# Performance work log

Measured on AMD Instinct MI355X. Metric: run time of the kernel, lower is better.

Reference implementation:

```python
import jax, jax.numpy as jnp
import numpy as np
from jax import lax

B, S, H, V, J, K = 8, 512, 768, 35004, 30, 9
PAD = 0

def setup_inputs() -> dict:
    key = jax.random.key(0)
    ks = jax.random.split(key, 12)
    std = 0.02
    return {
        'x': jax.random.randint(ks[0], (B, S), 0, V),
        'decoder_input': jax.random.normal(ks[1], (B, J, H), jnp.float32),
        'encoder_output': jax.random.normal(ks[2], (B, S, H), jnp.float32),
        'hidden': jax.random.normal(ks[3], (1, B, H), jnp.float32),
        'teacher': jax.random.randint(ks[4], (B, J, K), 0, V),
        'max_len': K,
        'embed': jax.random.normal(ks[5], (V, H), jnp.float32) * std,
        'w_ih': jax.random.normal(ks[6], (3 * H, H), jnp.float32) * std,
        'w_hh': jax.random.normal(ks[7], (3 * H, H), jnp.float32) * std,
        'b_ih': jnp.zeros((3 * H,), jnp.float32),
        'b_hh': jnp.zeros((3 * H,), jnp.float32),
        'wg_w': jax.random.normal(ks[8], (1, 3 * H), jnp.float32) * std,
        'wg_b': jnp.zeros((1,), jnp.float32),
    }

def gru_cell(w, h, w_ih, w_hh, b_ih, b_hh):
    # PyTorch GRU gate order: reset, update, new
    gi = w @ w_ih.T + b_ih          # [B,3H]
    gh = h @ w_hh.T + b_hh          # [B,3H]
    ir, iz, inn = jnp.split(gi, 3, axis=-1)
    hr, hz, hn = jnp.split(gh, 3, axis=-1)
    r = jax.nn.sigmoid(ir + hr)
    z = jax.nn.sigmoid(iz + hz)
    n = jnp.tanh(inn + r * hn)
    return (1.0 - z) * n + z * h

def reference(x, decoder_input, encoder_output, hidden, teacher, max_len,
              embed, w_ih, w_hh, b_ih, b_hh, wg_w, wg_b):
    mask = (x == PAD)                      # [B,S]
    batch_ix = jnp.arange(x.shape[0])[:, None]

    def tok_step(carry, teach_t):
        w, h = carry                       # w,h: [B,H]; teach_t: [B]
        h = gru_cell(w, h, w_ih, w_hh, b_ih, b_hh)
        logits_hist = jnp.einsum('bsh,bh->bs', encoder_output, h)
        logits_hist = jnp.where(mask, -1e9, logits_hist)
        a_hist = jax.nn.softmax(logits_hist, axis=-1)          # [B,S]
        a_vocab = jax.nn.softmax(h @ embed.T, axis=-1)         # [B,V]
        context = jnp.einsum('bs,bsh->bh', a_hist, encoder_output)
        p_gen = jax.nn.sigmoid(
            jnp.concatenate([w, h, context], axis=-1) @ wg_w.T + wg_b)  # [B,1]
        p_ctx = jnp.zeros_like(a_vocab).at[batch_ix, x].add(a_hist)     # scatter_add pointer copy
        p_final = p_gen * a_vocab + (1.0 - p_gen) * p_ctx
        w_next = embed[teach_t]            # teacher forcing (dropout omitted: eval mode)
        return (w_next, h), p_final

    def slot_step(h, slot_in):
        w0, teach_j = slot_in              # w0: [B,H]; teach_j: [K,B]
        (_, h), p = lax.scan(tok_step, (w0, h), teach_j)
        return h, p                        # p: [K,B,V]

    h0 = hidden[0]                                      # [B,H]
    slots = jnp.swapaxes(decoder_input, 0, 1)           # [J,B,H]
    teach = jnp.transpose(teacher, (1, 2, 0))           # [J,K,B]
    _, outs = lax.scan(slot_step, h0, (slots, teach))   # [J,K,B,V]
    return jnp.transpose(outs, (2, 0, 1, 3))            # [B,J,K,V]
```

## Files before the change

### kernel.cpp

```cpp
#include <hip/hip_runtime.h>
#include <hip/hip_bf16.h>

typedef _Float16 f16;
typedef _Float16 f16x8 __attribute__((ext_vector_type(8)));
typedef _Float16 h2 __attribute__((ext_vector_type(2)));
typedef float f32x4 __attribute__((ext_vector_type(4)));
typedef unsigned ui4v __attribute__((ext_vector_type(4)));
typedef unsigned long long ull;

#define B_ 8
#define S_ 512
#define H_ 768
#define V_ 35004
#define J_ 30
#define K_ 9
#define R_ 2160
#define H3 2304
#define CBLK 24
#define CUPB 32


__global__ void k_zero(int* p, int n) {
    int i = blockIdx.x * 256 + threadIdx.x;
    if (i < n) p[i] = 0;
}

__global__ void k_cast(const float* __restrict__ s, f16* __restrict__ d, long n) {
    for (long i = (long)blockIdx.x * 256 + threadIdx.x; i < n; i += (long)gridDim.x * 256)
        d[i] = (f16)s[i];
}

__global__ void k_build_wall(const float* __restrict__ emb, const float* __restrict__ dec,
                             const int* __restrict__ teacher, f16* __restrict__ Wall) {
    int r = blockIdx.x;
    int b = r / 270, s = r % 270, j = s / 9, t = s % 9;
    const float* src = (t == 0) ? dec + ((long)b * J_ + j) * H_
                                : emb + (long)teacher[((long)b * J_ + j) * K_ + (t - 1)] * H_;
    f16* dst = Wall + (long)r * H_;
    for (int c = threadIdx.x; c < H_; c += 256) dst[c] = (f16)src[c];
}

__global__ void k_build_enc(const float* __restrict__ enc, f16* __restrict__ ehi,
                            f16* __restrict__ elo, f16* __restrict__ encT) {
    long n = (long)B_ * S_ * H_;
    for (long i = (long)blockIdx.x * 256 + threadIdx.x; i < n; i += (long)gridDim.x * 256) {
        float v = enc[i];
        f16 hi = (f16)v;
        ehi[i] = hi;
        elo[i] = (f16)(v - (float)hi);
        int h = (int)(i % H_);
        long bs = i / H_;
        int s = (int)(bs % S_), b = (int)(bs / S_);
        encT[((long)b * H_ + h) * S_ + s] = hi;
    }
}

__global__ void k_init_h(const float* __restrict__ hidden, ull* __restrict__ hbuf) {
    int i = blockIdx.x * 256 + threadIdx.x;
    if (i < B_ * H_) {
        int b = i / H_, u = i % H_;
        hbuf[(long)b * 1536 + u] = (ull)__float_as_uint(hidden[i]);
    }
}

typedef const __attribute__((address_space(1))) unsigned GASU;
typedef __attribute__((address_space(3))) unsigned LASU;
__device__ __forceinline__ void gld16(const f16* g, f16* l) {
    __builtin_amdgcn_global_load_lds((GASU*)g, (LASU*)l, 16, 0, 0);
}

template <int MODE>
__global__ __launch_bounds__(256) void k_gemm(const f16* __restrict__ A, const f16* __restrict__ Bm,
                                              float* __restrict__ C, const float* __restrict__ bias,
                                              int M, int N, int K, long sA, long sB, long sC,
                                              float* __restrict__ psum) {
    A += (long)blockIdx.z * sA;
    Bm += (long)blockIdx.z * sB;
    C += (long)blockIdx.z * sC;
    const int m0 = blockIdx.y * 128, n0 = blockIdx.x * 128;
    __shared__ f16 As[128 * 32];
    __shared__ f16 Bs[128 * 32];
    __shared__ float rpart[2][128];
    const int tid = threadIdx.x, lane = tid & 63, wave = tid >> 6;
    const int wm = wave >> 1, wn = wave & 1;
    const int fr = lane & 15, kg = lane >> 4;
    f32x4 acc[4][4] = {};
    const int idxu = wave * 128;
    const int i0 = idxu + lane, i1 = idxu + 64 + lane;
    const int r0 = i0 >> 2, k80 = i0 & 3;
    const int r1 = i1 >> 2, k81 = i1 & 3;
    int ga0 = m0 + r0; if (ga0 >= M) ga0 = M - 1;
    int ga1 = m0 + r1; if (ga1 >= M) ga1 = M - 1;
    int gb0 = n0 + r0; if (gb0 >= N) gb0 = N - 1;
    int gb1 = n0 + r1; if (gb1 >= N) gb1 = N - 1;
    const f16* pa0 = A + (long)ga0 * K + k80 * 8;
    const f16* pa1 = A + (long)ga1 * K + k81 * 8;
    const f16* pb0 = Bm + (long)gb0 * K + k80 * 8;
    const f16* pb1 = Bm + (long)gb1 * K + k81 * 8;
    for (int kt = 0; kt < K; kt += 32) {
        gld16(pa0 + kt, As + idxu * 8);
        gld16(pa1 + kt, As + idxu * 8 + 512);
        gld16(pb0 + kt, Bs + idxu * 8);
        gld16(pb1 + kt, Bs + idxu * 8 + 512);
        __syncthreads();
        f16x8 af[4], bf[4];
#pragma unroll
        for (int m = 0; m < 4; ++m) af[m] = *(const f16x8*)(As + (wm * 64 + m * 16 + fr) * 32 + kg * 8);
#pragma unroll
        for (int n = 0; n < 4; ++n) bf[n] = *(const f16x8*)(Bs + (wn * 64 + n * 16 + fr) * 32 + kg * 8);
#pragma unroll
        for (int m = 0; m < 4; ++m)
#pragma unroll
            for (int n = 0; n < 4; ++n)
                acc[m][n] = __builtin_amdgcn_mfma_f32_16x16x32_f16(af[m], bf[n], acc[m][n], 0, 0, 0);
        __syncthreads();
    }
    const int crow = m0 + wm * 64 + (lane >> 4) * 4;
    const int ccol = n0 + wn * 64 + fr;
    if (MODE == 3) {
        float rs[4][4];
#pragma unroll
        for (int m = 0; m < 4; ++m)
#pragma unroll
            for (int q = 0; q < 4; ++q) rs[m][q] = 0.f;
#pragma unroll
        for (int n = 0; n < 4; ++n) {
            int col = ccol + n * 16;
            if (col >= N) continue;
#pragma unroll
            for (int m = 0; m < 4; ++m) {
#pragma unroll
                for (int q = 0; q < 4; ++q) {
                    int row = crow + m * 16 + q;
                    if (row < M) {
                        float e = __expf(acc[m][n][q]);
                        C[(long)row * N + col] = e;
                        rs[m][q] += e;
                    }
                }
            }
        }
#pragma unroll
        for (int m = 0; m < 4; ++m)
#pragma unroll
            for (int q = 0; q < 4; ++q) {
                float v = rs[m][q];
                v += __shfl_xor(v, 1);
                v += __shfl_xor(v, 2);
                v += __shfl_xor(v, 4);
                v += __shfl_xor(v, 8);
                rs[m][q] = v;
            }
        if ((lane & 15) == 0) {
#pragma unroll
            for (int m = 0; m < 4; ++m)
#pragma unroll
                for (int q = 0; q < 4; ++q)
                    rpart[wn][wm * 64 + (lane >> 4) * 4 + m * 16 + q] = rs[m][q];
        }
        __syncthreads();
        if (tid < 128) {
            int row = m0 + tid;
            if (row < M) psum[(long)blockIdx.x * M + row] = rpart[0][tid] + rpart[1][tid];
        }
    } else {
#pragma unroll
        for (int n = 0; n < 4; ++n) {
            int col = ccol + n * 16;
            if (col >= N) continue;
            float bv = (MODE == 1) ? bias[col] : 0.f;
#pragma unroll
            for (int m = 0; m < 4; ++m) {
#pragma unroll
                for (int q = 0; q < 4; ++q) {
                    int row = crow + m * 16 + q;
                    if (row < M) {
                        long idx = (long)row * N + col;
                        float v = acc[m][n][q] + bv;
                        if (MODE == 2) v += C[idx];
                        C[idx] = v;
                    }
                }
            }
        }
    }
}

__device__ __forceinline__ float fd2(unsigned hv, unsigned wv, float acc) {
#if __has_builtin(__builtin_amdgcn_fdot2)
    return __builtin_amdgcn_fdot2(__builtin_bit_cast(h2, hv), __builtin_bit_cast(h2, wv), acc, false);
#else
    h2 a = __builtin_bit_cast(h2, hv), b = __builtin_bit_cast(h2, wv);
    return acc + (float)a.x * (float)b.x + (float)a.y * (float)b.y;
#endif
}

__global__ __launch_bounds__(256, 1) void k_gru(const float* __restrict__ gi,
                                                const f16* __restrict__ wh16,
                                                const float* __restrict__ bhh,
                                                ull* hbuf,
                                                f16* __restrict__ Hhi, f16* __restrict__ Hlo) {
    __shared__ ui4v wsvu[9216];
    __shared__ __align__(16) f16 hsf[768];
    __shared__ float hs32[768];
    __shared__ float part[8][32][3];
    const int tid = threadIdx.x;
    const int chain = blockIdx.x / CBLK;
    const int blk = blockIdx.x % CBLK;
    const int u0 = blk * CUPB;
    for (int idx = tid; idx < 9216; idx += 256) {
        int uu = idx & 31, k8 = (idx >> 5) % 96, g = idx / (96 * 32);
        wsvu[idx] = *(const ui4v*)(wh16 + (long)(g * H_ + u0 + uu) * H_ + k8 * 8);
    }
    float b_r = 0.f, b_z = 0.f, b_n = 0.f;
    if (tid < 32) {
        int c = u0 + tid;
        b_r = bhh[c];
        b_z = bhh[H_ + c];
        b_n = bhh[2 * H_ + c];
    }
    __syncthreads();
    const int u = tid & 31, q = tid >> 5;
    ui4v wreg[3][12];
#pragma unroll
    for (int g = 0; g < 3; ++g)
#pragma unroll
        for (int i = 0; i < 12; ++i)
            wreg[g][i] = wsvu[(g * 96 + q * 12 + i) * 32 + u];
    ull* base = hbuf + (long)chain * 1536;
    for (int s = 0; s < 270; ++s) {
        const ull* rb = base + (s & 1) * 768;
        ull* wb = base + ((s + 1) & 1) * 768;
        const unsigned want = (unsigned)s;
        ull v0, v1, v2;
        for (;;) {
            v0 = __hip_atomic_load(rb + tid, __ATOMIC_RELAXED, __HIP_MEMORY_SCOPE_AGENT);
            v1 = __hip_atomic_load(rb + tid + 256, __ATOMIC_RELAXED, __HIP_MEMORY_SCOPE_AGENT);
            v2 = __hip_atomic_load(rb + tid + 512, __ATOMIC_RELAXED, __HIP_MEMORY_SCOPE_AGENT);
            bool ok = ((unsigned)(v0 >> 32) == want) & ((unsigned)(v1 >> 32) == want) &
                      ((unsigned)(v2 >> 32) == want);
            if (ok) break;
        }
        float f0 = __uint_as_float((unsigned)v0);
        float f1 = __uint_as_float((unsigned)v1);
        float f2 = __uint_as_float((unsigned)v2);
        hs32[tid] = f0;         hsf[tid] = (f16)f0;
        hs32[tid + 256] = f1;   hsf[tid + 256] = (f16)f1;
        hs32[tid + 512] = f2;   hsf[tid + 512] = (f16)f2;
        __syncthreads();
        float hold = 0.f, g0 = 0.f, g1 = 0.f, g2v = 0.f;
        if (tid < 32) {
            int c = u0 + tid;
            hold = hs32[c];
            const float* gp = gi + ((long)chain * 270 + s) * H3;
            g0 = gp[c];
            g1 = gp[H_ + c];
            g2v = gp[2 * H_ + c];
        }
        float ar = 0.f, az = 0.f, an = 0.f;
#pragma unroll
        for (int i = 0; i < 12; ++i) {
            ui4v hv = *(const ui4v*)(&hsf[(q * 12 + i) * 8]);
            ui4v wr = wreg[0][i], wz = wreg[1][i], wn = wreg[2][i];
            ar = fd2(hv.x, wr.x, ar); ar = fd2(hv.y, wr.y, ar);
            ar = fd2(hv.z, wr.z, ar); ar = fd2(hv.w, wr.w, ar);
            az = fd2(hv.x, wz.x, az); az = fd2(hv.y, wz.y, az);
            az = fd2(hv.z, wz.z, az); az = fd2(hv.w, wz.w, az);
            an = fd2(hv.x, wn.x, an); an = fd2(hv.y, wn.y, an);
            an = fd2(hv.z, wn.z, an); an = fd2(hv.w, wn.w, an);
        }
        part[q][u][0] = ar;
        part[q][u][1] = az;
        part[q][u][2] = an;
        __syncthreads();
        if (tid < 32) {
            float gr = b_r, gz = b_z, gn = b_n;
#pragma unroll
            for (int qq = 0; qq < 8; ++qq) {
                gr += part[qq][tid][0];
                gz += part[qq][tid][1];
                gn += part[qq][tid][2];
            }
            float rg = 1.f / (1.f + expf(-(g0 + gr)));
            float zg = 1.f / (1.f + expf(-(g1 + gz)));
            float ng = tanhf(g2v + rg * gn);
            float hnew = (1.f - zg) * ng + zg * hold;
            int c = u0 + tid;
            ull wv = ((ull)(unsigned)(s + 1) << 32) | (ull)__float_as_uint(hnew);
            __hip_atomic_store(wb + c, wv, __ATOMIC_RELAXED, __HIP_MEMORY_SCOPE_AGENT);
            long row = (long)chain * 270 + s;
            f16 hi16 = (f16)hnew;
            Hhi[row * H_ + c] = hi16;
            Hlo[row * H_ + c] = (f16)(hnew - (float)hi16);
        }
    }
}

__global__ __launch_bounds__(256) void k_attn_softmax(const float* __restrict__ lg,
                                                      const int* __restrict__ x, f16* __restrict__ ah) {
    __shared__ float red[256];
    int r = blockIdx.x, tid = threadIdx.x;
    int b = r / 270;
    const float* lr = lg + (long)r * S_;
    const int* xb = x + (long)b * S_;
    float v0 = lr[tid];
    if (xb[tid] == 0) v0 = -1e9f;
    float v1 = lr[tid + 256];
    if (xb[tid + 256] == 0) v1 = -1e9f;
    red[tid] = fmaxf(v0, v1);
    __syncthreads();
    for (int o = 128; o > 0; o >>= 1) {
        if (tid < o) red[tid] = fmaxf(red[tid], red[tid + o]);
        __syncthreads();
    }
    float m = red[0];
    __syncthreads();
    float e0 = __expf(v0 - m), e1 = __expf(v1 - m);
    red[tid] = e0 + e1;
    __syncthreads();
    for (int o = 128; o > 0; o >>= 1) {
        if (tid < o) red[tid] += red[tid + o];
        __syncthreads();
    }
    float inv = 1.f / red[0];
    ah[(long)r * S_ + tid] = (f16)(e0 * inv);
    ah[(long)r * S_ + tid + 256] = (f16)(e1 * inv);
}

__global__ __launch_bounds__(256) void k_pgen(const f16* __restrict__ Wall, const f16* __restrict__ Hhi,
                                              const f16* __restrict__ Hlo, const float* __restrict__ ctx,
                                              const float* __restrict__ wg, const float* __restrict__ wgb,
                                              float* __restrict__ pg) {
    __shared__ float red[256];
    int r = blockIdx.x, tid = threadIdx.x;
    float a = 0.f;
    for (int i = tid; i < H_; i += 256) {
        a += (float)Wall[(long)r * H_ + i] * wg[i];
        a += ((float)Hhi[(long)r * H_ + i] + (float)Hlo[(long)r * H_ + i]) * wg[H_ + i];
        a += ctx[(long)r * H_ + i] * wg[2 * H_ + i];
    }
    red[tid] = a;
    __syncthreads();
    for (int o = 128; o > 0; o >>= 1) {
        if (tid < o) red[tid] += red[tid + o];
        __syncthreads();
    }
    if (tid == 0) pg[r] = 1.f / (1.f + expf(-(red[0] + wgb[0])));
}

__global__ void k_redsum(const float* __restrict__ psum, float* __restrict__ rinv, int nb) {
    int r = blockIdx.x * 256 + threadIdx.x;
    if (r >= R_) return;
    float s = 0.f;
    for (int b = 0; b < nb; ++b) s += psum[(long)b * R_ + r];
    rinv[r] = 1.f / s;
}

__global__ __launch_bounds__(256) void k_final(float* __restrict__ out, const float* __restrict__ rinv,
                                               const float* __restrict__ pg) {
    int r = blockIdx.y;
    int i = blockIdx.x * 256 + threadIdx.x;
    if (i >= V_ / 4) return;
    float scale = pg[r] * rinv[r];
    f32x4* po = (f32x4*)(out + (long)r * V_);
    f32x4 v = po[i];
    v.x *= scale;
    v.y *= scale;
    v.z *= scale;
    v.w *= scale;
    po[i] = v;
}

__global__ __launch_bounds__(512) void k_scatter(float* __restrict__ out, const f16* __restrict__ ah,
                                                 const float* __restrict__ pg, const int* __restrict__ x) {
    int r = blockIdx.x, s = threadIdx.x;
    int b = r / 270;
    int xv = x[(long)b * S_ + s];
    if (xv == 0) return;
    float a = (float)ah[(long)r * S_ + s];
    if (a == 0.f) return;
    atomicAdd(out + (long)r * V_ + xv, (1.f - pg[r]) * a);
}

extern "C" void kernel_launch(void* const* d_in, const int* in_sizes, int n_in, void* d_out,
                              int out_size, void* d_ws, size_t ws_size, hipStream_t stream) {
    (void)in_sizes; (void)n_in; (void)out_size; (void)ws_size;
    const int* x = (const int*)d_in[0];
    const float* dec = (const float*)d_in[1];
    const float* enc = (const float*)d_in[2];
    const float* hid = (const float*)d_in[3];
    const int* tea = (const int*)d_in[4];
    const float* emb = (const float*)d_in[6];
    const float* wih = (const float*)d_in[7];
    const float* whh = (const float*)d_in[8];
    const float* bih = (const float*)d_in[9];
    const float* bhh = (const float*)d_in[10];
    const float* wgw = (const float*)d_in[11];
    const float* wgb = (const float*)d_in[12];
    float* out = (float*)d_out;

    char* w = (char*)d_ws;
    size_t off = 0;
    auto alloc = [&](size_t bytes) {
        void* p = w + off;
        off = (off + bytes + 255) & ~(size_t)255;
        return p;
    };
    ull* hbuf = (ull*)alloc(8 * 1536 * 8);
    f16* Wall = (f16*)alloc((size_t)R_ * H_ * 2);
    f16* wih16 = (f16*)alloc((size_t)H3 * H_ * 2);
    f16* wh16 = (f16*)alloc((size_t)H3 * H_ * 2);
    float* giA = (float*)alloc((size_t)R_ * H3 * 4);
    f16* Hhi = (f16*)alloc((size_t)R_ * H_ * 2);
    f16* Hlo = (f16*)alloc((size_t)R_ * H_ * 2);
    f16* emb16 = (f16*)alloc((size_t)V_ * H_ * 2);
    f16* ehi = (f16*)alloc((size_t)B_ * S_ * H_ * 2);
    f16* elo = (f16*)alloc((size_t)B_ * S_ * H_ * 2);
    f16* encT = (f16*)alloc((size_t)B_ * H_ * S_ * 2);
    float* lgH = (float*)alloc((size_t)R_ * S_ * 4);
    f16* ah = (f16*)alloc((size_t)R_ * S_ * 2);
    float* ctx = (float*)alloc((size_t)R_ * H_ * 4);
    float* pg = (float*)alloc(R_ * 4);
    float* psum = (float*)alloc((size_t)274 * R_ * 4);
    float* rinv = (float*)alloc(R_ * 4);

    const int nH = 8 * 1536 * 2;
    k_zero<<<(nH + 255) / 256, 256, 0, stream>>>((int*)hbuf, nH);
    k_cast<<<2048, 256, 0, stream>>>(emb, emb16, (long)V_ * H_);
    k_cast<<<512, 256, 0, stream>>>(wih, wih16, (long)H3 * H_);
    k_cast<<<512, 256, 0, stream>>>(whh, wh16, (long)H3 * H_);
    k_build_wall<<<R_, 256, 0, stream>>>(emb, dec, tea, Wall);
    k_build_enc<<<1024, 256, 0, stream>>>(enc, ehi, elo, encT);
    k_init_h<<<24, 256, 0, stream>>>(hid, hbuf);

    {
        dim3 g(H3 / 128, (R_ + 127) / 128, 1);
        k_gemm<1><<<g, 256, 0, stream>>>(Wall, wih16, giA, bih, R_, H3, H_, 0, 0, 0, nullptr);
    }
    k_gru<<<8 * CBLK, 256, 0, stream>>>(giA, wh16, bhh, hbuf, Hhi, Hlo);

    {
        dim3 g(S_ / 128, 3, 8);
        k_gemm<0><<<g, 256, 0, stream>>>(Hhi, ehi, lgH, nullptr, 270, S_, H_, 270L * H_, (long)S_ * H_, 270L * S_, nullptr);
        k_gemm<2><<<g, 256, 0, stream>>>(Hhi, elo, lgH, nullptr, 270, S_, H_, 270L * H_, (long)S_ * H_, 270L * S_, nullptr);
        k_gemm<2><<<g, 256, 0, stream>>>(Hlo, ehi, lgH, nullptr, 270, S_, H_, 270L * H_, (long)S_ * H_, 270L * S_, nullptr);
    }
    k_attn_softmax<<<R_, 256, 0, stream>>>(lgH, x, ah);
    {
        dim3 g(H_ / 128, 3, 8);
        k_gemm<0><<<g, 256, 0, stream>>>(ah, encT, ctx, nullptr, 270, H_, S_, 270L * S_, (long)H_ * S_, 270L * H_, nullptr);
    }
    k_pgen<<<R_, 256, 0, stream>>>(Wall, Hhi, Hlo, ctx, wgw, wgb, pg);

    {
        dim3 g((V_ + 127) / 128, (R_ + 127) / 128, 1);
        k_gemm<3><<<g, 256, 0, stream>>>(Hhi, emb16, out, nullptr, R_, V_, H_, 0, 0, 0, psum);
    }
    k_redsum<<<(R_ + 255) / 256, 256, 0, stream>>>(psum, rinv, (V_ + 127) / 128);
    {
        dim3 g((V_ / 4 + 255) / 256, R_, 1);
        k_final<<<g, 256, 0, stream>>>(out, rinv, pg);
    }
    k_scatter<<<R_, 512, 0, stream>>>(out, ah, pg, x);
}
```

Measured before the change: 1.221 ms.

## Fuse split-precision attention GEMMs and remap vocab GEMM tiles across XCDs

The three hi/lo attention-logit GEMM launches become one kernel that accumulates all three products in registers, so the two read-modify-write passes over the logits buffer go away. The vocab GEMM moves to a dedicated 1D-grid kernel that remaps workgroup IDs so each XCD gets a contiguous run of tiles. Within a run, consecutive tiles share the same embedding column block across the 17 row tiles, which should improve L2 reuse of the large fp16 embedding matrix. The cost is some duplicated GEMM code.

```diff
diff --git a/kernel.cpp b/kernel.cpp
--- a/kernel.cpp
+++ b/kernel.cpp
@@ -18,6 +18,8 @@
 #define H3 2304
 #define CBLK 24
 #define CUPB 32
+#define VMT 17
+#define VNT 274
 
 
 __global__ void k_zero(int* p, int n) {
@@ -72,12 +74,137 @@
 template <int MODE>
 __global__ __launch_bounds__(256) void k_gemm(const f16* __restrict__ A, const f16* __restrict__ Bm,
                                               float* __restrict__ C, const float* __restrict__ bias,
-                                              int M, int N, int K, long sA, long sB, long sC,
-                                              float* __restrict__ psum) {
+                                              int M, int N, int K, long sA, long sB, long sC) {
     A += (long)blockIdx.z * sA;
     Bm += (long)blockIdx.z * sB;
     C += (long)blockIdx.z * sC;
     const int m0 = blockIdx.y * 128, n0 = blockIdx.x * 128;
+    __shared__ f16 As[128 * 32];
+    __shared__ f16 Bs[128 * 32];
+    const int tid = threadIdx.x, lane = tid & 63, wave = tid >> 6;
+    const int wm = wave >> 1, wn = wave & 1;
+    const int fr = lane & 15, kg = lane >> 4;
+    f32x4 acc[4][4] = {};
+    const int idxu = wave * 128;
+    const int i0 = idxu + lane, i1 = idxu + 64 + lane;
+    const int r0 = i0 >> 2, k80 = i0 & 3;
+    const int r1 = i1 >> 2, k81 = i1 & 3;
+    int ga0 = m0 + r0; if (ga0 >= M) ga0 = M - 1;
+    int ga1 = m0 + r1; if (ga1 >= M) ga1 = M - 1;
+    int gb0 = n0 + r0; if (gb0 >= N) gb0 = N - 1;
+    int gb1 = n0 + r1; if (gb1 >= N) gb1 = N - 1;
+    const f16* pa0 = A + (long)ga0 * K + k80 * 8;
+    const f16* pa1 = A + (long)ga1 * K + k81 * 8;
+    const f16* pb0 = Bm + (long)gb0 * K + k80 * 8;
+    const f16* pb1 = Bm + (long)gb1 * K + k81 * 8;
+    for (int kt = 0; kt < K; kt += 32) {
+        gld16(pa0 + kt, As + idxu * 8);
+        gld16(pa1 + kt, As + idxu * 8 + 512);
+        gld16(pb0 + kt, Bs + idxu * 8);
+        gld16(pb1 + kt, Bs + idxu * 8 + 512);
+        __syncthreads();
+        f16x8 af[4], bf[4];
+#pragma unroll
+        for (int m = 0; m < 4; ++m) af[m] = *(const f16x8*)(As + (wm * 64 + m * 16 + fr) * 32 + kg * 8);
+#pragma unroll
+        for (int n = 0; n < 4; ++n) bf[n] = *(const f16x8*)(Bs + (wn * 64 + n * 16 + fr) * 32 + kg * 8);
+#pragma unroll
+        for (int m = 0; m < 4; ++m)
+#pragma unroll
+            for (int n = 0; n < 4; ++n)
+                acc[m][n] = __builtin_amdgcn_mfma_f32_16x16x32_f16(af[m], bf[n], acc[m][n], 0, 0, 0);
+        __syncthreads();
+    }
+    const int crow = m0 + wm * 64 + (lane >> 4) * 4;
+    const int ccol = n0 + wn * 64 + fr;
+#pragma unroll
+    for (int n = 0; n < 4; ++n) {
+        int col = ccol + n * 16;
+        if (col >= N) continue;
+        float bv = (MODE == 1) ? bias[col] : 0.f;
+#pragma unroll
+        for (int m = 0; m < 4; ++m) {
+#pragma unroll
+            for (int q = 0; q < 4; ++q) {
+                int row = crow + m * 16 + q;
+                if (row < M) C[(long)row * N + col] = acc[m][n][q] + bv;
+            }
+        }
+    }
+}
+
+__global__ __launch_bounds__(256) void k_attn3(const f16* __restrict__ Ahi, const f16* __restrict__ Alo,
+                                               const f16* __restrict__ Bhi, const f16* __restrict__ Blo,
+                                               float* __restrict__ C, int M, int N, int K,
+                                               long sA, long sB, long sC) {
+    const long za = (long)blockIdx.z * sA, zb = (long)blockIdx.z * sB;
+    C += (long)blockIdx.z * sC;
+    const int m0 = blockIdx.y * 128, n0 = blockIdx.x * 128;
+    __shared__ f16 As[128 * 32];
+    __shared__ f16 Bs[128 * 32];
+    const int tid = threadIdx.x, lane = tid & 63, wave = tid >> 6;
+    const int wm = wave >> 1, wn = wave & 1;
+    const int fr = lane & 15, kg = lane >> 4;
+    f32x4 acc[4][4] = {};
+    const int idxu = wave * 128;
+    const int i0 = idxu + lane, i1 = idxu + 64 + lane;
+    const int r0 = i0 >> 2, k80 = i0 & 3;
+    const int r1 = i1 >> 2, k81 = i1 & 3;
+    int ga0 = m0 + r0; if (ga0 >= M) ga0 = M - 1;
+    int ga1 = m0 + r1; if (ga1 >= M) ga1 = M - 1;
+    int gb0 = n0 + r0; if (gb0 >= N) gb0 = N - 1;
+    int gb1 = n0 + r1; if (gb1 >= N) gb1 = N - 1;
+    const long oa0 = (long)ga0 * K + k80 * 8, oa1 = (long)ga1 * K + k81 * 8;
+    const long ob0 = (long)gb0 * K + k80 * 8, ob1 = (long)gb1 * K + k81 * 8;
+    for (int ph = 0; ph < 3; ++ph) {
+        const f16* Ap = (ph == 2 ? Alo : Ahi) + za;
+        const f16* Bp = (ph == 1 ? Blo : Bhi) + zb;
+        for (int kt = 0; kt < K; kt += 32) {
+            gld16(Ap + oa0 + kt, As + idxu * 8);
+            gld16(Ap + oa1 + kt, As + idxu * 8 + 512);
+            gld16(Bp + ob0 + kt, Bs + idxu * 8);
+            gld16(Bp + ob1 + kt, Bs + idxu * 8 + 512);
+            __syncthreads();
+            f16x8 af[4], bf[4];
+#pragma unroll
+            for (int m = 0; m < 4; ++m) af[m] = *(const f16x8*)(As + (wm * 64 + m * 16 + fr) * 32 + kg * 8);
+#pragma unroll
+            for (int n = 0; n < 4; ++n) bf[n] = *(const f16x8*)(Bs + (wn * 64 + n * 16 + fr) * 32 + kg * 8);
+#pragma unroll
+            for (int m = 0; m < 4; ++m)
+#pragma unroll
+                for (int n = 0; n < 4; ++n)
+                    acc[m][n] = __builtin_amdgcn_mfma_f32_16x16x32_f16(af[m], bf[n], acc[m][n], 0, 0, 0);
+            __syncthreads();
+        }
+    }
+    const int crow = m0 + wm * 64 + (lane >> 4) * 4;
+    const int ccol = n0 + wn * 64 + fr;
+#pragma unroll
+    for (int n = 0; n < 4; ++n) {
+        int col = ccol + n * 16;
+        if (col >= N) continue;
+#pragma unroll
+        for (int m = 0; m < 4; ++m) {
+#pragma unroll
+            for (int q = 0; q < 4; ++q) {
+                int row = crow + m * 16 + q;
+                if (row < M) C[(long)row * N + col] = acc[m][n][q];
+            }
+        }
+    }
+}
+
+__global__ __launch_bounds__(256) void k_vocab(const f16* __restrict__ A, const f16* __restrict__ Bm,
+                                               float* __restrict__ C, float* __restrict__ psum) {
+    const int M = R_, N = V_, K = H_;
+    const int nwg = VMT * VNT;
+    int lin = blockIdx.x;
+    int q8 = nwg / 8, r8 = nwg % 8;
+    int xcd = lin & 7, idx = lin >> 3;
+    int newlin = (xcd < r8) ? xcd * (q8 + 1) + idx : r8 * (q8 + 1) + (xcd - r8) * q8 + idx;
+    int mt = newlin % VMT, nt = newlin / VMT;
+    const int m0 = mt * 128, n0 = nt * 128;
     __shared__ f16 As[128 * 32];
     __shared__ f16 Bs[128 * 32];
     __shared__ float rpart[2][128];
@@ -117,72 +244,50 @@
     }
     const int crow = m0 + wm * 64 + (lane >> 4) * 4;
     const int ccol = n0 + wn * 64 + fr;
-    if (MODE == 3) {
-        float rs[4][4];
-#pragma unroll
-        for (int m = 0; m < 4; ++m)
-#pragma unroll
-            for (int q = 0; q < 4; ++q) rs[m][q] = 0.f;
-#pragma unroll
-        for (int n = 0; n < 4; ++n) {
-            int col = ccol + n * 16;
-            if (col >= N) continue;
-#pragma unroll
-            for (int m = 0; m < 4; ++m) {
-#pragma unroll
-                for (int q = 0; q < 4; ++q) {
-                    int row = crow + m * 16 + q;
-                    if (row < M) {
-                        float e = __expf(acc[m][n][q]);
-                        C[(long)row * N + col] = e;
-                        rs[m][q] += e;
-                    }
+    float rs[4][4];
+#pragma unroll
+    for (int m = 0; m < 4; ++m)
+#pragma unroll
+        for (int q = 0; q < 4; ++q) rs[m][q] = 0.f;
+#pragma unroll
+    for (int n = 0; n < 4; ++n) {
+        int col = ccol + n * 16;
+        if (col >= N) continue;
+#pragma unroll
+        for (int m = 0; m < 4; ++m) {
+#pragma unroll
+            for (int q = 0; q < 4; ++q) {
+                int row = crow + m * 16 + q;
+                if (row < M) {
+                    float e = __expf(acc[m][n][q]);
+                    C[(long)row * N + col] = e;
+                    rs[m][q] += e;
                 }
             }
         }
+    }
+#pragma unroll
+    for (int m = 0; m < 4; ++m)
+#pragma unroll
+        for (int q = 0; q < 4; ++q) {
+            float v = rs[m][q];
+            v += __shfl_xor(v, 1);
+            v += __shfl_xor(v, 2);
+            v += __shfl_xor(v, 4);
+            v += __shfl_xor(v, 8);
+            rs[m][q] = v;
+        }
+    if ((lane & 15) == 0) {
 #pragma unroll
         for (int m = 0; m < 4; ++m)
 #pragma unroll
-            for (int q = 0; q < 4; ++q) {
-                float v = rs[m][q];
-                v += __shfl_xor(v, 1);
-                v += __shfl_xor(v, 2);
-                v += __shfl_xor(v, 4);
-                v += __shfl_xor(v, 8);
-                rs[m][q] = v;
-            }
-        if ((lane & 15) == 0) {
-#pragma unroll
-            for (int m = 0; m < 4; ++m)
-#pragma unroll
-                for (int q = 0; q < 4; ++q)
-                    rpart[wn][wm * 64 + (lane >> 4) * 4 + m * 16 + q] = rs[m][q];
-        }
-        __syncthreads();
-        if (tid < 128) {
-            int row = m0 + tid;
-            if (row < M) psum[(long)blockIdx.x * M + row] = rpart[0][tid] + rpart[1][tid];
-        }
-    } else {
-#pragma unroll
-        for (int n = 0; n < 4; ++n) {
-            int col = ccol + n * 16;
-            if (col >= N) continue;
-            float bv = (MODE == 1) ? bias[col] : 0.f;
-#pragma unroll
-            for (int m = 0; m < 4; ++m) {
-#pragma unroll
-                for (int q = 0; q < 4; ++q) {
-                    int row = crow + m * 16 + q;
-                    if (row < M) {
-                        long idx = (long)row * N + col;
-                        float v = acc[m][n][q] + bv;
-                        if (MODE == 2) v += C[idx];
-                        C[idx] = v;
-                    }
-                }
-            }
-        }
+            for (int q = 0; q < 4; ++q)
+                rpart[wn][wm * 64 + (lane >> 4) * 4 + m * 16 + q] = rs[m][q];
+    }
+    __syncthreads();
+    if (tid < 128) {
+        int row = m0 + tid;
+        if (row < M) psum[(long)nt * M + row] = rpart[0][tid] + rpart[1][tid];
     }
 }
 
@@ -421,7 +526,7 @@
     f16* ah = (f16*)alloc((size_t)R_ * S_ * 2);
     float* ctx = (float*)alloc((size_t)R_ * H_ * 4);
     float* pg = (float*)alloc(R_ * 4);
-    float* psum = (float*)alloc((size_t)274 * R_ * 4);
+    float* psum = (float*)alloc((size_t)VNT * R_ * 4);
     float* rinv = (float*)alloc(R_ * 4);
 
     const int nH = 8 * 1536 * 2;
@@ -435,28 +540,24 @@
 
     {
         dim3 g(H3 / 128, (R_ + 127) / 128, 1);
-        k_gemm<1><<<g, 256, 0, stream>>>(Wall, wih16, giA, bih, R_, H3, H_, 0, 0, 0, nullptr);
+        k_gemm<1><<<g, 256, 0, stream>>>(Wall, wih16, giA, bih, R_, H3, H_, 0, 0, 0);
     }
     k_gru<<<8 * CBLK, 256, 0, stream>>>(giA, wh16, bhh, hbuf, Hhi, Hlo);
 
     {
         dim3 g(S_ / 128, 3, 8);
-        k_gemm<0><<<g, 256, 0, stream>>>(Hhi, ehi, lgH, nullptr, 270, S_, H_, 270L * H_, (long)S_ * H_, 270L * S_, nullptr);
-        k_gemm<2><<<g, 256, 0, stream>>>(Hhi, elo, lgH, nullptr, 270, S_, H_, 270L * H_, (long)S_ * H_, 270L * S_, nullptr);
-        k_gemm<2><<<g, 256, 0, stream>>>(Hlo, ehi, lgH, nullptr, 270, S_, H_, 270L * H_, (long)S_ * H_, 270L * S_, nullptr);
+        k_attn3<<<g, 256, 0, stream>>>(Hhi, Hlo, ehi, elo, lgH, 270, S_, H_,
+                                       270L * H_, (long)S_ * H_, 270L * S_);
     }
     k_attn_softmax<<<R_, 256, 0, stream>>>(lgH, x, ah);
     {
         dim3 g(H_ / 128, 3, 8);
-        k_gemm<0><<<g, 256, 0, stream>>>(ah, encT, ctx, nullptr, 270, H_, S_, 270L * S_, (long)H_ * S_, 270L * H_, nullptr);
+        k_gemm<0><<<g, 256, 0, stream>>>(ah, encT, ctx, nullptr, 270, H_, S_, 270L * S_, (long)H_ * S_, 270L * H_);
     }
     k_pgen<<<R_, 256, 0, stream>>>(Wall, Hhi, Hlo, ctx, wgw, wgb, pg);
 
-    {
-        dim3 g((V_ + 127) / 128, (R_ + 127) / 128, 1);
-        k_gemm<3><<<g, 256, 0, stream>>>(Hhi, emb16, out, nullptr, R_, V_, H_, 0, 0, 0, psum);
-    }
-    k_redsum<<<(R_ + 255) / 256, 256, 0, stream>>>(psum, rinv, (V_ + 127) / 128);
+    k_vocab<<<VMT * VNT, 256, 0, stream>>>(Hhi, emb16, out, psum);
+    k_redsum<<<(R_ + 255) / 256, 256, 0, stream>>>(psum, rinv, VNT);
     {
         dim3 g((V_ / 4 + 255) / 256, R_, 1);
         k_final<<<g, 256, 0, stream>>>(out, rinv, pg);
```

Result: faster. 1.152 ms (-5.6%).
